# Kernel optimization log

Hardware: AMD Instinct MI355X
Metric: run time of the kernel (lower is better)

Reference implementation:

```python
import jax, jax.numpy as jnp
import numpy as np

B = 4096          # batch of vectors
D = 768           # embedding_size
P = 96            # partition (number of sub-quantizers)
C = 256           # centroids per partition
SD = D // P       # sub-vector dim = 8


def setup_inputs() -> dict:
    key = jax.random.key(0)
    k1, k2 = jax.random.split(key)
    vecs = jax.random.normal(k1, (B, D), dtype=jnp.float32)
    # nn.Parameter(torch.empty(P, C, SD).uniform_(-0.1, 0.1))
    codebook = jax.random.uniform(k2, (P, C, SD), dtype=jnp.float32,
                                  minval=-0.1, maxval=0.1)
    return {"vecs": vecs, "codebook": codebook}


def _quantize(vecs, codebook):
    # vecs: [B, D] -> [B, P, SD]
    v = vecs.reshape(vecs.shape[0], P, SD)
    # proba = -sum((v - c)^2) expanded to avoid the [B,P,C,SD] intermediate:
    # ||v||^2 - 2 v.c + ||c||^2  per (b, p, c)
    v_sq = jnp.sum(v * v, axis=-1, keepdims=True)            # [B, P, 1]
    c_sq = jnp.sum(codebook * codebook, axis=-1)             # [P, C]
    vc = jnp.einsum('bpd,pcd->bpc', v, codebook)             # [B, P, C]
    proba = -(v_sq - 2.0 * vc + c_sq[None])                  # [B, P, C]
    assign = jax.nn.softmax(proba, axis=-1)                  # [B, P, C]
    # straight-through estimator: hard one-hot fwd, soft grad
    index = jnp.argmax(assign, axis=-1)                      # [B, P]
    assign_hard = jax.nn.one_hot(index, C, dtype=assign.dtype)
    assign_ste = jax.lax.stop_gradient(assign_hard - assign) + assign
    # reconstruction: [B,P,C] @ [P,C,SD] -> [B,P,SD] -> [B,D]
    q = jnp.einsum('bpc,pcd->bpd', assign_ste, codebook)
    return q.reshape(vecs.shape[0], -1)


def reference(vecs, codebook):
    return _quantize(vecs, codebook)
```

## Files before the change

### kernel.cpp

```cpp
#include <hip/hip_runtime.h>
#include <cmath>

constexpr int B  = 4096;
constexpr int D  = 768;
constexpr int P  = 96;
constexpr int C  = 256;
constexpr int SD = 8;

constexpr int TPB   = 192;
constexpr int PT    = 3;
constexpr int RT    = 256;
constexpr int ROWS  = 4;
constexpr int VROW  = 28;

__device__ __forceinline__ float tree8(float q0, float q1, float q2, float q3,
                                       float q4, float q5, float q6, float q7)
{
#pragma clang fp contract(off)
    return ((q0 + q1) + (q2 + q3)) + ((q4 + q5) + (q6 + q7));
}

__device__ __forceinline__ float proba_np(const float* __restrict__ cbf,
                                          const float* __restrict__ csq,
                                          int c, float4 va, float4 vb, float vsq)
{
#pragma clang fp contract(off)
    float4 ca = ((const float4*)cbf)[2 * c];
    float4 cb = ((const float4*)cbf)[2 * c + 1];
    float p0 = va.x * ca.x, p1 = va.y * ca.y, p2 = va.z * ca.z, p3 = va.w * ca.w;
    float p4 = vb.x * cb.x, p5 = vb.y * cb.y, p6 = vb.z * cb.z, p7 = vb.w * cb.w;
    float l0 = p0 + p4, l1 = p1 + p5, l2 = p2 + p6, l3 = p3 + p7;
    float vc = (l0 + l2) + (l1 + l3);
    float tt = vsq - 2.0f * vc;
    float u  = tt + csq[c];
    return -u;
}

__device__ __attribute__((noinline))
int exact_search(const float* __restrict__ cbf, const float* __restrict__ csq,
                 float4 va, float4 vb, float vsq)
{
#pragma clang fp contract(off)
    float best = -3.402823466e38f, second = -3.402823466e38f;
    int bi = 0;
    for (int c = 0; c < C; ++c) {
        float pr = proba_np(cbf, csq, c, va, vb, vsq);
        if (pr > best)        { second = best; best = pr; bi = c; }
        else if (pr > second) { second = pr; }
    }
    int idx = bi;

    if (best - second <= 1.0e-6f) {
        float m = best;
        float r0[8] = {0,0,0,0,0,0,0,0};
        float r1[8] = {0,0,0,0,0,0,0,0};
        for (int cg = 0; cg < 16; ++cg) {
            #pragma unroll
            for (int j = 0; j < 8; ++j) {
                float pr = proba_np(cbf, csq, cg * 8 + j, va, vb, vsq);
                r0[j] += expf(pr - m);
            }
        }
        for (int cg = 16; cg < 32; ++cg) {
            #pragma unroll
            for (int j = 0; j < 8; ++j) {
                float pr = proba_np(cbf, csq, cg * 8 + j, va, vb, vsq);
                r1[j] += expf(pr - m);
            }
        }
        float sum = tree8(r0[0],r0[1],r0[2],r0[3],r0[4],r0[5],r0[6],r0[7])
                  + tree8(r1[0],r1[1],r1[2],r1[3],r1[4],r1[5],r1[6],r1[7]);
        float abest = -1.0f;
        int   ai    = 0;
        for (int c = 0; c < C; ++c) {
            float pr = proba_np(cbf, csq, c, va, vb, vsq);
            float e  = expf(pr - m);
            float a  = e / sum;
            if (a > abest) { abest = a; ai = c; }
        }
        idx = ai;
    }
    return idx;
}

__global__ __launch_bounds__(TPB, 4)
void pq_coal_kernel(const float* __restrict__ vecs,
                    const float* __restrict__ codebook,
                    float* __restrict__ out)
{
    __shared__ float vt  [RT * VROW];
    __shared__ float cbl [PT * C * SD];
    __shared__ float csqn[PT * C];
    __shared__ float csqh[PT * C];

    const int t  = threadIdx.x;
    const int w  = t >> 6;
    const int l  = t & 63;
    const int bx = blockIdx.x;
    const int rowbase = blockIdx.y * RT;
    const int t6  = t / 6;
    const int tm6 = t - 6 * t6;

    {
        const float4* src = (const float4*)(codebook + (size_t)(3 * bx) * C * SD);
        float4* dst = (float4*)cbl;
        #pragma unroll
        for (int k = 0; k < 8; ++k)
            dst[t + TPB * k] = src[t + TPB * k];
    }
    {
        const float4* src = (const float4*)vecs;
        #pragma unroll
        for (int k = 0; k < 8; ++k) {
            int row = k * 32 + t6;
            float4 x = src[(size_t)(rowbase + row) * (D / 4) + bx * 6 + tm6];
            *(float4*)(vt + row * VROW + tm6 * 4) = x;
        }
    }
    __syncthreads();

    #pragma unroll
    for (int k = 0; k < 4; ++k) {
        int c = t + TPB * k;
        const float* cc = cbl + c * SD;
        float q0 = cc[0]*cc[0], q1 = cc[1]*cc[1], q2 = cc[2]*cc[2], q3 = cc[3]*cc[3];
        float q4 = cc[4]*cc[4], q5 = cc[5]*cc[5], q6 = cc[6]*cc[6], q7 = cc[7]*cc[7];
        float s = tree8(q0,q1,q2,q3,q4,q5,q6,q7);
        csqn[c] = s;
        csqh[c] = -0.5f * s;
    }

    float4 va[ROWS], vb[ROWS];
    #pragma unroll
    for (int r = 0; r < ROWS; ++r) {
        const float* vp = vt + (64 * r + l) * VROW + w * SD;
        va[r] = *(const float4*)(vp);
        vb[r] = *(const float4*)(vp + 4);
    }
    __syncthreads();

    const float4* CB = (const float4*)(cbl + w * C * SD);
    const float*  CH = csqh + w * C;

    float best[ROWS], second[ROWS];
    int   bi[ROWS];
    #pragma unroll
    for (int r = 0; r < ROWS; ++r) {
        best[r] = -3.402823466e38f; second[r] = -3.402823466e38f; bi[r] = 0;
    }

    for (int c = 0; c < C; c += 4) {
        float4 A[4], Bv[4];
        float  H[4];
        #pragma unroll
        for (int u = 0; u < 4; ++u) {
            A[u]  = CB[2 * (c + u)];
            Bv[u] = CB[2 * (c + u) + 1];
            H[u]  = CH[c + u];
        }
        #pragma unroll
        for (int u = 0; u < 4; ++u) {
            #pragma unroll
            for (int r = 0; r < ROWS; ++r) {
                float s = fmaf(va[r].x, A[u].x, H[u]);
                s = fmaf(va[r].y, A[u].y, s);
                s = fmaf(va[r].z, A[u].z, s);
                s = fmaf(va[r].w, A[u].w, s);
                s = fmaf(vb[r].x, Bv[u].x, s);
                s = fmaf(vb[r].y, Bv[u].y, s);
                s = fmaf(vb[r].z, Bv[u].z, s);
                s = fmaf(vb[r].w, Bv[u].w, s);
                bool gt = s > best[r];
                second[r] = fmaxf(second[r], fminf(s, best[r]));
                bi[r]     = gt ? (c + u) : bi[r];
                best[r]   = fmaxf(s, best[r]);
            }
        }
    }

    const float* cbf_w = cbl + w * C * SD;
    const float* csq_w = csqn + w * C;
    #pragma unroll
    for (int r = 0; r < ROWS; ++r) {
        int idx = bi[r];
        if (best[r] - second[r] <= 2.0e-5f) {
            float q0 = va[r].x*va[r].x, q1 = va[r].y*va[r].y,
                  q2 = va[r].z*va[r].z, q3 = va[r].w*va[r].w;
            float q4 = vb[r].x*vb[r].x, q5 = vb[r].y*vb[r].y,
                  q6 = vb[r].z*vb[r].z, q7 = vb[r].w*vb[r].w;
            float vsq = tree8(q0,q1,q2,q3,q4,q5,q6,q7);
            idx = exact_search(cbf_w, csq_w, va[r], vb[r], vsq);
        }
        float4 o0 = ((const float4*)cbf_w)[2 * idx];
        float4 o1 = ((const float4*)cbf_w)[2 * idx + 1];
        float* op = vt + (64 * r + l) * VROW + w * SD;
        *(float4*)(op)     = o0;
        *(float4*)(op + 4) = o1;
    }
    __syncthreads();

    {
        float4* dst = (float4*)out;
        #pragma unroll
        for (int k = 0; k < 8; ++k) {
            int row = k * 32 + t6;
            float4 x = *(const float4*)(vt + row * VROW + tm6 * 4);
            dst[(size_t)(rowbase + row) * (D / 4) + bx * 6 + tm6] = x;
        }
    }
}

extern "C" void kernel_launch(void* const* d_in, const int* in_sizes, int n_in,
                              void* d_out, int out_size, void* d_ws, size_t ws_size,
                              hipStream_t stream)
{
    const float* vecs     = (const float*)d_in[0];
    const float* codebook = (const float*)d_in[1];
    float*       out      = (float*)d_out;

    dim3 grid(P / PT, B / RT);
    dim3 block(TPB);
    pq_coal_kernel<<<grid, block, 0, stream>>>(vecs, codebook, out);
}
```

Measured before the change: 191.7 us.

## Split centroid search across wave pairs and merge partial argmax in shared memory

Each block now covers 2 partitions with 4 waves, and each pair of waves splits the 256 centroids into halves. The partial best, second-best and index values are merged through shared memory. This gives a larger grid and shorter per-thread loops. The shared-memory staging of vecs and output tiles is dropped: vectors are loaded directly from global memory with 32-byte strided accesses, and outputs are written directly. The trade-off is less coalesced global traffic, an extra reduction and sync step, and a lower launch-bounds occupancy hint.

Result: slower. 221.1 us (+15.4%).

```diff
diff --git a/kernel.cpp b/kernel.cpp
--- a/kernel.cpp
+++ b/kernel.cpp
@@ -7,11 +7,9 @@
 constexpr int C  = 256;
 constexpr int SD = 8;
 
-constexpr int TPB   = 192;
-constexpr int PT    = 3;
-constexpr int RT    = 256;
-constexpr int ROWS  = 4;
-constexpr int VROW  = 28;
+constexpr int TPB  = 256;
+constexpr int ROWS = 4;
+constexpr int CH2  = C / 2;
 
 __device__ __forceinline__ float tree8(float q0, float q1, float q2, float q3,
                                        float q4, float q5, float q6, float q7)
@@ -83,45 +81,37 @@
     return idx;
 }
 
-__global__ __launch_bounds__(TPB, 4)
-void pq_coal_kernel(const float* __restrict__ vecs,
-                    const float* __restrict__ codebook,
-                    float* __restrict__ out)
-{
-    __shared__ float vt  [RT * VROW];
-    __shared__ float cbl [PT * C * SD];
-    __shared__ float csqn[PT * C];
-    __shared__ float csqh[PT * C];
+__global__ __launch_bounds__(TPB, 3)
+void pq_bal_kernel(const float* __restrict__ vecs,
+                   const float* __restrict__ codebook,
+                   float* __restrict__ out)
+{
+    __shared__ float  cbl [2 * C * SD];
+    __shared__ float  csqn[2 * C];
+    __shared__ float  csqh[2 * C];
+    __shared__ float2 part_bs[4][256];
+    __shared__ int    part_i [4][256];
 
     const int t  = threadIdx.x;
     const int w  = t >> 6;
     const int l  = t & 63;
+    const int p_loc  = w >> 1;
+    const int c_half = w & 1;
     const int bx = blockIdx.x;
-    const int rowbase = blockIdx.y * RT;
-    const int t6  = t / 6;
-    const int tm6 = t - 6 * t6;
+    const int rowbase = blockIdx.y * 256;
 
     {
-        const float4* src = (const float4*)(codebook + (size_t)(3 * bx) * C * SD);
+        const float4* src = (const float4*)(codebook + (size_t)(2 * bx) * C * SD);
         float4* dst = (float4*)cbl;
         #pragma unroll
-        for (int k = 0; k < 8; ++k)
-            dst[t + TPB * k] = src[t + TPB * k];
-    }
-    {
-        const float4* src = (const float4*)vecs;
-        #pragma unroll
-        for (int k = 0; k < 8; ++k) {
-            int row = k * 32 + t6;
-            float4 x = src[(size_t)(rowbase + row) * (D / 4) + bx * 6 + tm6];
-            *(float4*)(vt + row * VROW + tm6 * 4) = x;
-        }
+        for (int k = 0; k < 4; ++k)
+            dst[t + 256 * k] = src[t + 256 * k];
     }
     __syncthreads();
 
     #pragma unroll
-    for (int k = 0; k < 4; ++k) {
-        int c = t + TPB * k;
+    for (int k = 0; k < 2; ++k) {
+        int c = t + 256 * k;
         const float* cc = cbl + c * SD;
         float q0 = cc[0]*cc[0], q1 = cc[1]*cc[1], q2 = cc[2]*cc[2], q3 = cc[3]*cc[3];
         float q4 = cc[4]*cc[4], q5 = cc[5]*cc[5], q6 = cc[6]*cc[6], q7 = cc[7]*cc[7];
@@ -129,18 +119,19 @@
         csqn[c] = s;
         csqh[c] = -0.5f * s;
     }
-
+    __syncthreads();
+
+    const int p = 2 * bx + p_loc;
     float4 va[ROWS], vb[ROWS];
     #pragma unroll
     for (int r = 0; r < ROWS; ++r) {
-        const float* vp = vt + (64 * r + l) * VROW + w * SD;
-        va[r] = *(const float4*)(vp);
-        vb[r] = *(const float4*)(vp + 4);
-    }
-    __syncthreads();
-
-    const float4* CB = (const float4*)(cbl + w * C * SD);
-    const float*  CH = csqh + w * C;
+        const float* vptr = vecs + (size_t)(rowbase + 64 * r + l) * D + (size_t)p * SD;
+        va[r] = ((const float4*)vptr)[0];
+        vb[r] = ((const float4*)vptr)[1];
+    }
+
+    const float4* CB = (const float4*)(cbl + p_loc * C * SD);
+    const float*  CH = csqh + p_loc * C;
 
     float best[ROWS], second[ROWS];
     int   bi[ROWS];
@@ -149,15 +140,16 @@
         best[r] = -3.402823466e38f; second[r] = -3.402823466e38f; bi[r] = 0;
     }
 
-    for (int c = 0; c < C; c += 4) {
+    const int c0 = c_half * CH2;
+    for (int c = c0; c < c0 + CH2; c += 4) {
         float4 A[4], Bv[4];
-        float  H[4];
         #pragma unroll
         for (int u = 0; u < 4; ++u) {
             A[u]  = CB[2 * (c + u)];
             Bv[u] = CB[2 * (c + u) + 1];
-            H[u]  = CH[c + u];
-        }
+        }
+        float4 H4 = *(const float4*)(CH + c);
+        float H[4] = { H4.x, H4.y, H4.z, H4.w };
         #pragma unroll
         for (int u = 0; u < 4; ++u) {
             #pragma unroll
@@ -178,35 +170,44 @@
         }
     }
 
-    const float* cbf_w = cbl + w * C * SD;
-    const float* csq_w = csqn + w * C;
     #pragma unroll
     for (int r = 0; r < ROWS; ++r) {
-        int idx = bi[r];
-        if (best[r] - second[r] <= 2.0e-5f) {
-            float q0 = va[r].x*va[r].x, q1 = va[r].y*va[r].y,
-                  q2 = va[r].z*va[r].z, q3 = va[r].w*va[r].w;
-            float q4 = vb[r].x*vb[r].x, q5 = vb[r].y*vb[r].y,
-                  q6 = vb[r].z*vb[r].z, q7 = vb[r].w*vb[r].w;
+        part_bs[w][64 * r + l] = make_float2(best[r], second[r]);
+        part_i [w][64 * r + l] = bi[r];
+    }
+    __syncthreads();
+
+    #pragma unroll
+    for (int j = 0; j < 2; ++j) {
+        float2 b0 = part_bs[2 * j][t];
+        float2 b1 = part_bs[2 * j + 1][t];
+        int    i0 = part_i [2 * j][t];
+        int    i1 = part_i [2 * j + 1][t];
+
+        bool  gt  = b1.x > b0.x;
+        float Bst = fmaxf(b0.x, b1.x);
+        float Snd = fmaxf(fmaxf(b0.y, b1.y), fminf(b0.x, b1.x));
+        int   I   = gt ? i1 : i0;
+
+        const int row = rowbase + t;
+        const int pj  = 2 * bx + j;
+        int idx = I;
+        if (Bst - Snd <= 2.0e-5f) {
+            const float* vptr = vecs + (size_t)row * D + (size_t)pj * SD;
+            float4 xa = ((const float4*)vptr)[0];
+            float4 xb = ((const float4*)vptr)[1];
+            float q0 = xa.x*xa.x, q1 = xa.y*xa.y, q2 = xa.z*xa.z, q3 = xa.w*xa.w;
+            float q4 = xb.x*xb.x, q5 = xb.y*xb.y, q6 = xb.z*xb.z, q7 = xb.w*xb.w;
             float vsq = tree8(q0,q1,q2,q3,q4,q5,q6,q7);
-            idx = exact_search(cbf_w, csq_w, va[r], vb[r], vsq);
-        }
-        float4 o0 = ((const float4*)cbf_w)[2 * idx];
-        float4 o1 = ((const float4*)cbf_w)[2 * idx + 1];
-        float* op = vt + (64 * r + l) * VROW + w * SD;
-        *(float4*)(op)     = o0;
-        *(float4*)(op + 4) = o1;
-    }
-    __syncthreads();
-
-    {
-        float4* dst = (float4*)out;
-        #pragma unroll
-        for (int k = 0; k < 8; ++k) {
-            int row = k * 32 + t6;
-            float4 x = *(const float4*)(vt + row * VROW + tm6 * 4);
-            dst[(size_t)(rowbase + row) * (D / 4) + bx * 6 + tm6] = x;
-        }
+            idx = exact_search(cbl + j * C * SD, csqn + j * C, xa, xb, vsq);
+        }
+
+        const float4* cbw = (const float4*)(cbl + j * C * SD);
+        float4 o0 = cbw[2 * idx];
+        float4 o1 = cbw[2 * idx + 1];
+        float4* op = (float4*)(out + (size_t)row * D + (size_t)pj * SD);
+        op[0] = o0;
+        op[1] = o1;
     }
 }
 
@@ -218,7 +219,7 @@
     const float* codebook = (const float*)d_in[1];
     float*       out      = (float*)d_out;
 
-    dim3 grid(P / PT, B / RT);
+    dim3 grid(P / 2, B / 256);
     dim3 block(TPB);
-    pq_coal_kernel<<<grid, block, 0, stream>>>(vecs, codebook, out);
-}
+    pq_bal_kernel<<<grid, block, 0, stream>>>(vecs, codebook, out);
+}
```
